# Kernel tuning notes

Hardware: AMD Instinct MI355X
Metric: run time of the kernel (lower is better)

## Reference

```python
import jax, jax.numpy as jnp
import numpy as np

K = 16  # number of neighbors (init kwarg k)


def setup_inputs() -> dict:
    key = jax.random.key(0)
    k1, k2 = jax.random.split(key)
    B, N, D, F = 2, 2048, 16, 64
    points = jax.random.normal(k1, (B, N, D), dtype=jnp.float32)
    features = jax.random.normal(k2, (B, N, F), dtype=jnp.float32)
    return {"features": features, "points": points}


def reference(features, points):
    # points: [B, N, D]
    B, N, _ = points.shape
    # Pairwise Euclidean distances via broadcasted subtraction, matching
    # tf.norm(points[:, :, None] - points[:, None, :], axis=-1): [B, N, N]
    diff = points[:, :, None, :] - points[:, None, :, :]
    distance = jnp.sqrt(jnp.sum(diff * diff, axis=-1))
    # top (k+1) smallest distances == top_k of negated distance; drop self (col 0)
    _, topk_indices = jax.lax.top_k(-distance, K + 1)  # [B, N, K+1] int32
    topk_indices = topk_indices[:, :, 1:]               # [B, N, K]
    batch_indices = jnp.broadcast_to(
        jnp.arange(B, dtype=jnp.int32)[:, None, None, None], (B, N, K, 1)
    )
    # [B, N, K, 2] -> (batch_idx, neighbor_idx) pairs for gather_nd-style use
    return jnp.concatenate([batch_indices, topk_indices[..., None]], axis=3)
```

## Files before the change

kernel.cpp:

```cpp
#include <hip/hip_runtime.h>
#include <stdint.h>


#define NPTS 2048
#define DIMS 16
#define KK 16
#define THREADS 128
#define CPL 16

__device__ __forceinline__ void ce(uint64_t& a, uint64_t& b) {
    uint64_t lo = (a < b) ? a : b;
    uint64_t hi = (a < b) ? b : a;
    a = lo; b = hi;
}

__device__ __forceinline__ uint64_t wave_min_u64(uint64_t v) {
    uint32_t lo = (uint32_t)v;
    uint32_t hi = (uint32_t)(v >> 32);
#define DPP_STEP(CTRL, RMASK)                                                   \
    {                                                                           \
        uint32_t slo = (uint32_t)__builtin_amdgcn_update_dpp(                   \
            -1, (int)lo, (CTRL), (RMASK), 0xF, false);                          \
        uint32_t shi = (uint32_t)__builtin_amdgcn_update_dpp(                   \
            -1, (int)hi, (CTRL), (RMASK), 0xF, false);                          \
        bool lt = (shi < hi) || ((shi == hi) && (slo < lo));                    \
        lo = lt ? slo : lo;                                                     \
        hi = lt ? shi : hi;                                                     \
    }
    DPP_STEP(0x111, 0xF);
    DPP_STEP(0x112, 0xF);
    DPP_STEP(0x114, 0xF);
    DPP_STEP(0x118, 0xF);
    DPP_STEP(0x142, 0xA);
    DPP_STEP(0x143, 0xC);
#undef DPP_STEP
    uint32_t glo = (uint32_t)__builtin_amdgcn_readlane((int)lo, 63);
    uint32_t ghi = (uint32_t)__builtin_amdgcn_readlane((int)hi, 63);
    return ((uint64_t)ghi << 32) | glo;
}

__global__ __launch_bounds__(THREADS, 4) void knn_kernel(
    const float* __restrict__ points, int* __restrict__ out)
{
    const int q = blockIdx.x;
    const int b = q >> 11;
    const int n = q & (NPTS - 1);
    const float* bp = points + (size_t)b * NPTS * DIMS;

    __shared__ uint64_t lists[2][KK + 1];

    const int tid = threadIdx.x;
    const int wave = tid >> 6;
    const int lane = tid & 63;

    float qp[DIMS];
    {
        const float4* qp4 = (const float4*)(bp + (size_t)n * DIMS);
#pragma unroll
        for (int v = 0; v < 4; ++v) {
            float4 t = qp4[v];
            qp[4 * v + 0] = t.x; qp[4 * v + 1] = t.y;
            qp[4 * v + 2] = t.z; qp[4 * v + 3] = t.w;
        }
    }

    uint64_t k[CPL];
#pragma unroll
    for (int j = 0; j < CPL; ++j) {
        const int c = (wave << 10) + lane + (j << 6);
        const float4* cp4 = (const float4*)(bp + (size_t)c * DIMS);
        float s[DIMS];
#pragma unroll
        for (int v = 0; v < 4; ++v) {
            float4 t = cp4[v];
            float d0 = qp[4 * v + 0] - t.x;
            float d1 = qp[4 * v + 1] - t.y;
            float d2_ = qp[4 * v + 2] - t.z;
            float d3 = qp[4 * v + 3] - t.w;
            s[4 * v + 0] = __fmul_rn(d0, d0);
            s[4 * v + 1] = __fmul_rn(d1, d1);
            s[4 * v + 2] = __fmul_rn(d2_, d2_);
            s[4 * v + 3] = __fmul_rn(d3, d3);
        }
        float r0 = __fadd_rn(s[0], s[8]);
        float r1 = __fadd_rn(s[1], s[9]);
        float r2 = __fadd_rn(s[2], s[10]);
        float r3 = __fadd_rn(s[3], s[11]);
        float r4 = __fadd_rn(s[4], s[12]);
        float r5 = __fadd_rn(s[5], s[13]);
        float r6 = __fadd_rn(s[6], s[14]);
        float r7 = __fadd_rn(s[7], s[15]);
        float t0 = __fadd_rn(r0, r1);
        float t1 = __fadd_rn(r2, r3);
        float t2 = __fadd_rn(r4, r5);
        float t3 = __fadd_rn(r6, r7);
        float d2 = __fadd_rn(__fadd_rn(t0, t1), __fadd_rn(t2, t3));
        float dist = __fsqrt_rn(d2);
        k[j] = ((uint64_t)__float_as_uint(dist) << 32) | (uint32_t)c;
    }

#pragma unroll
    for (int r = 0; r < 2; ++r) {
        uint64_t* p = k + r * 8;
        ce(p[0], p[1]); ce(p[2], p[3]); ce(p[4], p[5]); ce(p[6], p[7]);
        ce(p[0], p[2]); ce(p[1], p[3]); ce(p[4], p[6]); ce(p[5], p[7]);
        ce(p[1], p[2]); ce(p[5], p[6]);
        ce(p[0], p[4]); ce(p[1], p[5]); ce(p[2], p[6]); ce(p[3], p[7]);
        ce(p[1], p[4]); ce(p[3], p[6]);
        ce(p[2], p[4]); ce(p[3], p[5]);
        ce(p[3], p[4]);
    }

    for (int r = 0; r <= KK; ++r) {
        const bool a_min = k[0] < k[8];
        const uint64_t m = a_min ? k[0] : k[8];
        const uint64_t g = wave_min_u64(m);
        if (m == g) {
            lists[wave][r] = g;
            if (a_min) {
#pragma unroll
                for (int j = 0; j < 7; ++j) k[j] = k[j + 1];
                k[7] = ~0ull;
            } else {
#pragma unroll
                for (int j = 8; j < 15; ++j) k[j] = k[j + 1];
                k[15] = ~0ull;
            }
        }
    }
    __syncthreads();

    if (lane <= KK) {
        const uint64_t mine = lists[wave][lane];
        const uint64_t* other = lists[wave ^ 1];
        int cnt = 0;
#pragma unroll
        for (int t = 0; t <= KK; ++t) cnt += (other[t] < mine) ? 1 : 0;
        const int rank = lane + cnt;
        if (rank >= 1 && rank <= KK) {
            int2 val;
            val.x = b;
            val.y = (int)(uint32_t)(mine & 0xffffffffu);
            *(int2*)(out + (((size_t)q * KK) + (size_t)(rank - 1)) * 2) = val;
        }
    }
}

extern "C" void kernel_launch(void* const* d_in, const int* in_sizes, int n_in,
                              void* d_out, int out_size, void* d_ws, size_t ws_size,
                              hipStream_t stream) {
    (void)d_ws; (void)ws_size; (void)out_size;
    const float* points;
    if (n_in >= 2 && in_sizes[1] == 2 * 2048 * 16) {
        points = (const float*)d_in[1];
    } else if (n_in >= 1 && in_sizes[0] == 2 * 2048 * 16) {
        points = (const float*)d_in[0];
    } else {
        points = (const float*)d_in[n_in - 1];
    }
    int* out = (int*)d_out;
    knn_kernel<<<2 * 2048, THREADS, 0, stream>>>(points, out);
}
```

Measured before the change: 94.28 us.

## Assign one query per wavefront and drop cross-wave shared-memory merge

Each wavefront now handles a whole query over all 2048 candidates (32 per lane), so a block of two waves processes two queries and the grid is halved. The shared-memory list merge and __syncthreads are removed. Self is excluded by masking c==n instead of extracting K+1 entries and dropping the first, and results are written directly from the selection loop. The cost is doubled register state per lane (launch bounds lowered to 2), partial unrolling of the distance loop, and a four-way min before each wave reduction. Masking by index instead of dropping the smallest entry can differ from the reference when a duplicate point sits at distance zero.

```diff
diff --git a/kernel.cpp b/kernel.cpp
--- a/kernel.cpp
+++ b/kernel.cpp
@@ -6,7 +6,7 @@
 #define DIMS 16
 #define KK 16
 #define THREADS 128
-#define CPL 16
+#define CPL 32
 
 __device__ __forceinline__ void ce(uint64_t& a, uint64_t& b) {
     uint64_t lo = (a < b) ? a : b;
@@ -39,19 +39,16 @@
     return ((uint64_t)ghi << 32) | glo;
 }
 
-__global__ __launch_bounds__(THREADS, 4) void knn_kernel(
+__global__ __launch_bounds__(THREADS, 2) void knn_kernel(
     const float* __restrict__ points, int* __restrict__ out)
 {
-    const int q = blockIdx.x;
+    const int tid = threadIdx.x;
+    const int wave = tid >> 6;
+    const int lane = tid & 63;
+    const int q = blockIdx.x * 2 + wave;
     const int b = q >> 11;
     const int n = q & (NPTS - 1);
     const float* bp = points + (size_t)b * NPTS * DIMS;
-
-    __shared__ uint64_t lists[2][KK + 1];
-
-    const int tid = threadIdx.x;
-    const int wave = tid >> 6;
-    const int lane = tid & 63;
 
     float qp[DIMS];
     {
@@ -65,9 +62,9 @@
     }
 
     uint64_t k[CPL];
-#pragma unroll
+#pragma unroll 4
     for (int j = 0; j < CPL; ++j) {
-        const int c = (wave << 10) + lane + (j << 6);
+        const int c = lane + (j << 6);
         const float4* cp4 = (const float4*)(bp + (size_t)c * DIMS);
         float s[DIMS];
 #pragma unroll
@@ -96,11 +93,12 @@
         float t3 = __fadd_rn(r6, r7);
         float d2 = __fadd_rn(__fadd_rn(t0, t1), __fadd_rn(t2, t3));
         float dist = __fsqrt_rn(d2);
-        k[j] = ((uint64_t)__float_as_uint(dist) << 32) | (uint32_t)c;
+        uint64_t key = ((uint64_t)__float_as_uint(dist) << 32) | (uint32_t)c;
+        k[j] = (c == n) ? ~0ull : key;
     }
 
 #pragma unroll
-    for (int r = 0; r < 2; ++r) {
+    for (int r = 0; r < 4; ++r) {
         uint64_t* p = k + r * 8;
         ce(p[0], p[1]); ce(p[2], p[3]); ce(p[4], p[5]); ce(p[6], p[7]);
         ce(p[0], p[2]); ce(p[1], p[3]); ce(p[4], p[6]); ce(p[5], p[7]);
@@ -111,37 +109,34 @@
         ce(p[3], p[4]);
     }
 
-    for (int r = 0; r <= KK; ++r) {
-        const bool a_min = k[0] < k[8];
-        const uint64_t m = a_min ? k[0] : k[8];
+    for (int r = 0; r < KK; ++r) {
+        uint64_t m = k[0]; int hm = 0;
+        if (k[8]  < m) { m = k[8];  hm = 1; }
+        if (k[16] < m) { m = k[16]; hm = 2; }
+        if (k[24] < m) { m = k[24]; hm = 3; }
         const uint64_t g = wave_min_u64(m);
         if (m == g) {
-            lists[wave][r] = g;
-            if (a_min) {
+            int2 val;
+            val.x = b;
+            val.y = (int)(uint32_t)(g & 0xffffffffu);
+            *(int2*)(out + (((size_t)q * KK) + (size_t)r) * 2) = val;
+            if (hm == 0) {
 #pragma unroll
                 for (int j = 0; j < 7; ++j) k[j] = k[j + 1];
                 k[7] = ~0ull;
-            } else {
+            } else if (hm == 1) {
 #pragma unroll
                 for (int j = 8; j < 15; ++j) k[j] = k[j + 1];
                 k[15] = ~0ull;
+            } else if (hm == 2) {
+#pragma unroll
+                for (int j = 16; j < 23; ++j) k[j] = k[j + 1];
+                k[23] = ~0ull;
+            } else {
+#pragma unroll
+                for (int j = 24; j < 31; ++j) k[j] = k[j + 1];
+                k[31] = ~0ull;
             }
-        }
-    }
-    __syncthreads();
-
-    if (lane <= KK) {
-        const uint64_t mine = lists[wave][lane];
-        const uint64_t* other = lists[wave ^ 1];
-        int cnt = 0;
-#pragma unroll
-        for (int t = 0; t <= KK; ++t) cnt += (other[t] < mine) ? 1 : 0;
-        const int rank = lane + cnt;
-        if (rank >= 1 && rank <= KK) {
-            int2 val;
-            val.x = b;
-            val.y = (int)(uint32_t)(mine & 0xffffffffu);
-            *(int2*)(out + (((size_t)q * KK) + (size_t)(rank - 1)) * 2) = val;
         }
     }
 }
@@ -159,5 +154,5 @@
         points = (const float*)d_in[n_in - 1];
     }
     int* out = (int*)d_out;
-    knn_kernel<<<2 * 2048, THREADS, 0, stream>>>(points, out);
+    knn_kernel<<<(2 * 2048) / 2, THREADS, 0, stream>>>(points, out);
 }
```

Result: slower. 123.3 us (+30.8%).
